# Performance work log

Hardware: AMD Instinct MI355X
Metric: run time of the kernel (lower is better)

The kernel has to match this reference:

```python
import jax, jax.numpy as jnp
import numpy as np

D = 512
HEADS = 4
DIM_HEAD = 128
SCALE = DIM_HEAD ** -0.5
A_NUMS = 60
N_NUMS = 60
DEPTH = 2


def _layer_norm(x, g, b, eps=1e-5):
    m = jnp.mean(x, axis=-1, keepdims=True)
    v = jnp.var(x, axis=-1, keepdims=True)
    return (x - m) * jax.lax.rsqrt(v + eps) * g + b


def _attention(x, qkv_w, out_w, out_b):
    B, T, _ = x.shape
    qkv = x @ qkv_w  # [B,T,3*H*Dh]
    q, k, v = jnp.split(qkv, 3, axis=-1)
    to_heads = lambda t: t.reshape(B, T, HEADS, DIM_HEAD).transpose(0, 2, 1, 3)
    q, k, v = to_heads(q), to_heads(k), to_heads(v)
    att = jax.nn.softmax(jnp.einsum('bhid,bhjd->bhij', q, k) * SCALE, axis=-1)
    o = jnp.einsum('bhij,bhjd->bhid', att, v).transpose(0, 2, 1, 3).reshape(B, T, HEADS * DIM_HEAD)
    return o @ out_w + out_b


def _memory(x, mem, nums):
    # sigmoid similarity to memory slots, topk-mean temporal score, weighted readout
    att = jax.nn.sigmoid(jnp.einsum('btd,kd->btk', x, mem) / jnp.sqrt(jnp.float32(D)))
    vals, _ = jax.lax.top_k(att, nums // 16 + 1)
    temporal_att = vals.mean(-1)  # [B,T]
    aug = jnp.einsum('btk,kd->btd', att, mem)
    return temporal_att, aug


def _topk_gather_mean(att, feats, k):
    _, idx = jax.lax.top_k(att, k)  # [B,k]
    g = jnp.take_along_axis(feats, idx[:, :, None], axis=1)  # [B,k,D]
    return g.mean(1), idx


def _l2norm(x):
    return x / jnp.linalg.norm(x, axis=-1, keepdims=True)


def setup_inputs():
    key = jax.random.key(0)
    ks = jax.random.split(key, 12)
    b, t, din = 64, 256, 1024
    s = 0.02
    return {
        'x': jax.random.normal(ks[0], (b, t, din), jnp.float32),
        'epsilon': jax.random.normal(ks[1], (b // 2, t, D), jnp.float32),
        'conv_w': jax.random.normal(ks[2], (D, din, 3), jnp.float32) * s,
        'conv_b': jnp.zeros((D,), jnp.float32),
        'ln1_g': jnp.ones((DEPTH, D), jnp.float32),
        'ln1_b': jnp.zeros((DEPTH, D), jnp.float32),
        'qkv_w': jax.random.normal(ks[3], (DEPTH, D, 3 * HEADS * DIM_HEAD), jnp.float32) * s,
        'out_w': jax.random.normal(ks[4], (DEPTH, HEADS * DIM_HEAD, D), jnp.float32) * s,
        'out_b': jnp.zeros((DEPTH, D), jnp.float32),
        'ln2_g': jnp.ones((DEPTH, D), jnp.float32),
        'ln2_b': jnp.zeros((DEPTH, D), jnp.float32),
        'ff1_w': jax.random.normal(ks[5], (DEPTH, D, D), jnp.float32) * s,
        'ff1_b': jnp.zeros((DEPTH, D), jnp.float32),
        'ff2_w': jax.random.normal(ks[6], (DEPTH, D, D), jnp.float32) * s,
        'ff2_b': jnp.zeros((DEPTH, D), jnp.float32),
        'a_mem': jax.random.normal(ks[7], (A_NUMS, D), jnp.float32) * s,
        'n_mem': jax.random.normal(ks[8], (N_NUMS, D), jnp.float32) * s,
        'mu_w': jax.random.normal(ks[9], (D, D), jnp.float32) * s,
        'mu_b': jnp.zeros((D,), jnp.float32),
        'var_w': jax.random.normal(ks[10], (D, D), jnp.float32) * s,
        'var_b': jnp.zeros((D,), jnp.float32),
    }


def reference(x, epsilon, conv_w, conv_b, ln1_g, ln1_b, qkv_w, out_w, out_b,
              ln2_g, ln2_b, ff1_w, ff1_b, ff2_w, ff2_b, a_mem, n_mem,
              mu_w, mu_b, var_w, var_b):
    b, t, _ = x.shape
    # Temporal embedding: Conv1d(k=3, pad=1) + ReLU
    h = jax.lax.conv_general_dilated(x.transpose(0, 2, 1), conv_w, (1,), [(1, 1)],
                                     dimension_numbers=('NCH', 'OIH', 'NCH'))
    h = jax.nn.relu(h + conv_b[None, :, None]).transpose(0, 2, 1)  # [B,T,512]
    # Transformer: PreNorm attn + PreNorm FF, residual, depth=2
    for i in range(DEPTH):
        h = h + _attention(_layer_norm(h, ln1_g[i], ln1_b[i]), qkv_w[i], out_w[i], out_b[i])
        f = _layer_norm(h, ln2_g[i], ln2_b[i])
        f = jax.nn.gelu(f @ ff1_w[i] + ff1_b[i], approximate=False)
        h = h + f @ ff2_w[i] + ff2_b[i]
    x_emb = h
    v_feat = x_emb.transpose(0, 2, 1)
    half = b // 2
    N_x, A_x = x_emb[:half], x_emb[half:]
    A_att, A_aug = _memory(A_x, a_mem, A_NUMS)
    N_Aatt, N_Aaug = _memory(A_x, n_mem, N_NUMS)
    A_Natt, A_Naug = _memory(N_x, a_mem, A_NUMS)
    N_att, N_aug = _memory(N_x, n_mem, N_NUMS)
    k = t // 16 + 1
    negative_ax, A_idx = _topk_gather_mean(A_att, A_x, k)
    anchor_nx, N_idx = _topk_gather_mean(N_att, N_x, k)
    positive_nx, _ = _topk_gather_mean(N_Aatt, A_x, k)
    eps = 1e-6
    an, ap, ng = _l2norm(anchor_nx), _l2norm(positive_nx), _l2norm(negative_ax)
    dp = jnp.linalg.norm(an - ap + eps, axis=-1)
    dn = jnp.linalg.norm(an - ng + eps, axis=-1)
    triplet = jnp.mean(jax.nn.relu(dp - dn + 1.0))
    N_aug_mu = N_aug @ mu_w + mu_b
    N_aug_var = N_aug @ var_w + var_b
    N_aug_new = N_aug_mu + epsilon * jnp.sqrt(jnp.exp(N_aug_var))
    anchor_nx_new = jnp.take_along_axis(N_aug_new, N_idx[:, :, None], axis=1).mean(1)
    A_aug_new = A_aug @ mu_w + mu_b
    negative_ax_new = jnp.take_along_axis(A_aug_new, A_idx[:, :, None], axis=1).mean(1)
    kl_loss = jnp.mean(-0.5 * jnp.sum(1.0 + N_aug_var - N_aug_mu ** 2 - jnp.exp(N_aug_var), axis=1))
    A_Naug_m = A_Naug @ mu_w + mu_b
    N_Aaug_m = N_Aaug @ mu_w + mu_b
    na = jnp.maximum(jnp.linalg.norm(anchor_nx, axis=1), eps)
    nn_ = jnp.maximum(jnp.linalg.norm(negative_ax, axis=1), eps)
    cos_loss = jnp.mean(1.0 - jnp.sum(anchor_nx * negative_ax, axis=1) / (na * nn_))
    distance = jnp.mean(jax.nn.relu(100.0 - jnp.linalg.norm(negative_ax_new, axis=-1)
                                    + jnp.linalg.norm(anchor_nx_new, axis=-1)))
    aug_cat = jnp.concatenate([N_aug_new + A_Naug_m, A_aug_new + N_Aaug_m], axis=0)
    x_out = jnp.concatenate([x_emb, aug_cat], axis=-1)  # [B,T,1024]
    return (triplet, kl_loss, distance, A_att, N_att, A_Natt, N_Aatt, cos_loss, x_out, v_feat)
```

## Files before the change

kernel.cpp:

```cpp
#include <hip/hip_runtime.h>
#include <math.h>

namespace {

typedef unsigned short u16;
typedef __attribute__((ext_vector_type(8))) short s8v;
typedef __attribute__((ext_vector_type(8))) unsigned short u16x8;
typedef __attribute__((ext_vector_type(4))) unsigned short u16x4;
typedef __attribute__((ext_vector_type(4))) float f32x4;
typedef __attribute__((ext_vector_type(4))) unsigned int u32x4;

constexpr int HBT = 8192;
constexpr long HHf = 4194304;

constexpr long F_H    = 0;
constexpr long F_LNB  = 8388608;
constexpr long F_QKV  = 12582912;
constexpr long F_VT   = 25165824;
constexpr long F_SC   = 29360128;
constexpr long F_ATT  = 12582912;
constexpr long F_AUG  = 14548992;
constexpr long F_MU   = 22937600;
constexpr long F_VAR  = 27131904;
constexpr long F_R0   = 31326208;
constexpr long F_R1   = 35520512;
constexpr long F_R2   = 39714816;
constexpr long W_MEMB = 43909120;
constexpr long Z_PG   = 43974656;
constexpr long W_QKV  = 46137344;
constexpr long W_OUT  = 46923776;
constexpr long W_FF1  = 47185920;
constexpr long W_FF2  = 47448064;
constexpr long W_MU   = 47710208;
constexpr long W_VAR  = 47841280;
constexpr long W_CONV = 47972352;
constexpr long W_AMT  = 48758784;
constexpr long W_NMT  = 48775168;
constexpr long O_ANC  = 48791552;
constexpr long O_POS  = O_ANC + 16384;
constexpr long O_NEG  = O_POS + 16384;
constexpr long O_ANEW = O_NEG + 16384;
constexpr long O_NNEG = O_ANEW + 16384;
constexpr long O_IDX  = O_NNEG + 16384;
constexpr long O_ACC  = O_IDX + 1632;

constexpr long OO_AATT  = 3;
constexpr long OO_NATT  = 3 + 8192;
constexpr long OO_ANATT = 3 + 16384;
constexpr long OO_NAATT = 3 + 24576;
constexpr long OO_COS   = 32771;
constexpr long OO_XOUT  = 32772;
constexpr long OO_VFEAT = 32772L + 16777216L;

__device__ inline u16 to_bf16(float f) {
  union { float f; unsigned u; } x; x.f = f;
  unsigned r = x.u + 0x7fffu + ((x.u >> 16) & 1u);
  return (u16)(r >> 16);
}
__device__ inline u16x8 pack8(float4 a, float4 b) {
  u16x8 r;
  r[0]=to_bf16(a.x); r[1]=to_bf16(a.y); r[2]=to_bf16(a.z); r[3]=to_bf16(a.w);
  r[4]=to_bf16(b.x); r[5]=to_bf16(b.y); r[6]=to_bf16(b.z); r[7]=to_bf16(b.w);
  return r;
}

typedef __attribute__((address_space(1))) void gvoid;
typedef __attribute__((address_space(3))) void lvoid;
__device__ inline void gld16(const u16* g, u16* l) {
  __builtin_amdgcn_global_load_lds((gvoid*)g, (lvoid*)l, 16, 0, 0);
}

__device__ inline float bred_sum(float v, float* sm, int tid) {
  sm[tid] = v; __syncthreads();
  for (int s = 128; s > 0; s >>= 1) { if (tid < s) sm[tid] += sm[tid + s]; __syncthreads(); }
  float r = sm[0]; __syncthreads();
  return r;
}

struct GP2 {
  const void* A; const void* B; const float* bias; void* C;
  const float* bias2;
  int M, N, K, lda, ldb, ldc, Hdiv;
  long sAb, sAh, sBb, sBh, sCb, sCh;
  float scale;
};


template<int EPI, bool ABF, bool BBF, bool ACC, bool CBF, bool GL>
__global__ __launch_bounds__(256) void mgemm_k(GP2 p) {
  __shared__ __align__(16) u16 As[4096];
  __shared__ __align__(16) u16 Bs[4096];
  int bb = blockIdx.z / p.Hdiv, hh = blockIdx.z % p.Hdiv;
  long aoff = (long)bb * p.sAb + (long)hh * p.sAh;
  long boff = (long)bb * p.sBb + (long)hh * p.sBh;
  long coff = (long)bb * p.sCb + (long)hh * p.sCh;
  int m0 = blockIdx.x * 128, n0 = blockIdx.y * 128;
  int tid = threadIdx.x, r = tid & 127, seg = tid >> 7;
  int lane = tid & 63, wave = tid >> 6;
  int wm = (wave >> 1) * 64, wn = (wave & 1) * 64;
  int l15 = lane & 15, quad = lane >> 4;
  int rs = (r >> 1) & 3;
  int qs = (quad ^ ((l15 >> 1) & 3)) * 8;
  f32x4 acc[4][4] = {};
  for (int k0 = 0; k0 < p.K; k0 += 32) {
    if constexpr (GL) {
      int lr = lane >> 2;
      int lc = (((lane & 3) ^ ((lane >> 3) & 3)) * 8);
      const u16* Ab = (const u16*)p.A + aoff + (long)(m0 + wave * 16 + lr) * p.lda + k0 + lc;
      gld16(Ab,                    &As[wave * 512]);
      gld16(Ab + (long)64 * p.lda, &As[2048 + wave * 512]);
      const u16* Bb = (const u16*)p.B + boff + (long)(n0 + wave * 16 + lr) * p.ldb + k0 + lc;
      gld16(Bb,                    &Bs[wave * 512]);
      gld16(Bb + (long)64 * p.ldb, &Bs[2048 + wave * 512]);
    } else {
      bool kfull = (k0 + 32 <= p.K);
      int p0 = ((2 * seg) ^ rs) * 8;
      int p1 = ((2 * seg + 1) ^ rs) * 8;
      {
        int gm = m0 + r;
        if (ABF) {
          const u16* Ar = (const u16*)p.A + aoff + (long)gm * p.lda + k0 + seg * 16;
          if (kfull) {
            *(u32x4*)&As[r * 32 + p0] = *(const u32x4*)Ar;
            *(u32x4*)&As[r * 32 + p1] = *(const u32x4*)(Ar + 8);
          } else {
            for (int c = 0; c < 16; c++) {
              int kk = k0 + seg * 16 + c;
              int cc = seg * 16 + c;
              As[r * 32 + (((cc >> 3) ^ rs) << 3) + (cc & 7)] = (kk < p.K) ? Ar[c] : (u16)0;
            }
          }
        } else {
          const float* Ar = (const float*)p.A + aoff + (long)gm * p.lda + k0 + seg * 16;
          if (kfull) {
            float4 f0 = ((const float4*)Ar)[0];
            float4 f1 = ((const float4*)Ar)[1];
            float4 f2 = ((const float4*)Ar)[2];
            float4 f3 = ((const float4*)Ar)[3];
            *(u16x8*)&As[r * 32 + p0] = pack8(f0, f1);
            *(u16x8*)&As[r * 32 + p1] = pack8(f2, f3);
          } else {
            for (int c = 0; c < 16; c++) {
              int kk = k0 + seg * 16 + c;
              int cc = seg * 16 + c;
              As[r * 32 + (((cc >> 3) ^ rs) << 3) + (cc & 7)] = (kk < p.K) ? to_bf16(Ar[c]) : (u16)0;
            }
          }
        }
      }
      {
        int gn = n0 + r;
        bool nv = gn < p.N;
        if (BBF) {
          const u16* Br = (const u16*)p.B + boff + (long)gn * p.ldb + k0 + seg * 16;
          if (nv && kfull) {
            *(u32x4*)&Bs[r * 32 + p0] = *(const u32x4*)Br;
            *(u32x4*)&Bs[r * 32 + p1] = *(const u32x4*)(Br + 8);
          } else {
            for (int c = 0; c < 16; c++) {
              int kk = k0 + seg * 16 + c;
              int cc = seg * 16 + c;
              Bs[r * 32 + (((cc >> 3) ^ rs) << 3) + (cc & 7)] = (nv && kk < p.K) ? Br[c] : (u16)0;
            }
          }
        } else {
          const float* Br = (const float*)p.B + boff + (long)gn * p.ldb + k0 + seg * 16;
          if (nv && kfull) {
            float4 f0 = ((const float4*)Br)[0];
            float4 f1 = ((const float4*)Br)[1];
            float4 f2 = ((const float4*)Br)[2];
            float4 f3 = ((const float4*)Br)[3];
            *(u16x8*)&Bs[r * 32 + p0] = pack8(f0, f1);
            *(u16x8*)&Bs[r * 32 + p1] = pack8(f2, f3);
          } else {
            for (int c = 0; c < 16; c++) {
              int kk = k0 + seg * 16 + c;
              int cc = seg * 16 + c;
              Bs[r * 32 + (((cc >> 3) ^ rs) << 3) + (cc & 7)] = (nv && kk < p.K) ? to_bf16(Br[c]) : (u16)0;
            }
          }
        }
      }
    }
    __syncthreads();
    s8v af[4], bfr[4];
#pragma unroll
    for (int i = 0; i < 4; i++) af[i]  = *(const s8v*)&As[(wm + i * 16 + l15) * 32 + qs];
#pragma unroll
    for (int j = 0; j < 4; j++) bfr[j] = *(const s8v*)&Bs[(wn + j * 16 + l15) * 32 + qs];
#pragma unroll
    for (int i = 0; i < 4; i++)
#pragma unroll
      for (int j = 0; j < 4; j++)
        acc[i][j] = __builtin_amdgcn_mfma_f32_16x16x32_bf16(af[i], bfr[j], acc[i][j], 0, 0, 0);
    __syncthreads();
  }
  const float* bp = (p.bias2 && (hh & 1)) ? p.bias2 : p.bias;
#pragma unroll
  for (int j = 0; j < 4; j++) {
    int col = n0 + wn + j * 16 + l15;
    if (col >= p.N) continue;
    float bv = bp ? bp[col] : 0.f;
#pragma unroll
    for (int i = 0; i < 4; i++) {
#pragma unroll
      for (int rr = 0; rr < 4; rr++) {
        int row = m0 + wm + i * 16 + quad * 4 + rr;
        float v = acc[i][j][rr] * p.scale + bv;
        if (EPI == 1) v = 0.5f * v * (1.f + erff(v * 0.70710678118654752f));
        if (EPI == 2) v = 1.f / (1.f + expf(-v));
        long ci = coff + (long)row * p.ldc + col;
        if (CBF) ((u16*)p.C)[ci] = to_bf16(v);
        else {
          float* Cp = (float*)p.C;
          if (ACC) v += Cp[ci];
          Cp[ci] = v;
        }
      }
    }
  }
}

__global__ __launch_bounds__(256) void convm_k(const u16* __restrict__ xb,
    const u16* __restrict__ zp, const u16* __restrict__ wT,
    const float* __restrict__ bias, float* __restrict__ out) {
  __shared__ __align__(16) u16 As[4096];
  __shared__ __align__(16) u16 Bs[4096];
  int m0 = blockIdx.x * 128, n0 = blockIdx.y * 128;
  int b = m0 >> 8, tb = m0 & 255;
  int tid = threadIdx.x;
  int lane = tid & 63, wave = tid >> 6;
  int wm = (wave >> 1) * 64, wn = (wave & 1) * 64;
  int l15 = lane & 15, quad = lane >> 4;
  int lr = lane >> 2;
  int lc = (((lane & 3) ^ ((lane >> 3) & 3)) * 8);
  int qs = (quad ^ ((l15 >> 1) & 3)) * 8;
  int arow = wave * 16 + lr;
  f32x4 acc[4][4] = {};
  for (int k0 = 0; k0 < 3072; k0 += 32) {
    int kp = k0 >> 10, i0 = (k0 & 1023);
    int t2a = tb + arow + kp - 1;
    const u16* Aa = (t2a >= 0 && t2a < 256)
        ? xb + ((long)(b * 256 + t2a)) * 1024 + i0 + lc
        : zp + lc;
    gld16(Aa, &As[wave * 512]);
    int t2b = t2a + 64;
    const u16* Ab2 = (t2b >= 0 && t2b < 256)
        ? xb + ((long)(b * 256 + t2b)) * 1024 + i0 + lc
        : zp + lc;
    gld16(Ab2, &As[2048 + wave * 512]);
    const u16* Bb = wT + (long)(n0 + arow) * 3072 + k0 + lc;
    gld16(Bb,                   &Bs[wave * 512]);
    gld16(Bb + (long)64 * 3072, &Bs[2048 + wave * 512]);
    __syncthreads();
    s8v af[4], bfr[4];
#pragma unroll
    for (int i = 0; i < 4; i++) af[i]  = *(const s8v*)&As[(wm + i * 16 + l15) * 32 + qs];
#pragma unroll
    for (int j = 0; j < 4; j++) bfr[j] = *(const s8v*)&Bs[(wn + j * 16 + l15) * 32 + qs];
#pragma unroll
    for (int i = 0; i < 4; i++)
#pragma unroll
      for (int j = 0; j < 4; j++)
        acc[i][j] = __builtin_amdgcn_mfma_f32_16x16x32_bf16(af[i], bfr[j], acc[i][j], 0, 0, 0);
    __syncthreads();
  }
#pragma unroll
  for (int j = 0; j < 4; j++) {
    int col = n0 + wn + j * 16 + l15;
    float bv = bias[col];
#pragma unroll
    for (int i = 0; i < 4; i++)
#pragma unroll
      for (int rr = 0; rr < 4; rr++) {
        int row = m0 + wm + i * 16 + quad * 4 + rr;
        float v = acc[i][j][rr] + bv;
        out[(long)row * 512 + col] = v > 0.f ? v : 0.f;
      }
  }
}

__global__ __launch_bounds__(256) void wtrans_k(const float* __restrict__ src,
    u16* __restrict__ dst, int R, int C) {
  __shared__ float t[32][33];
  int c0 = blockIdx.x * 32, r0 = blockIdx.y * 32;
  int tx = threadIdx.x & 31, ty = threadIdx.x >> 5;
  for (int rr = 0; rr < 32; rr += 8)
    t[ty + rr][tx] = src[(long)(r0 + ty + rr) * C + c0 + tx];
  __syncthreads();
  for (int rr = 0; rr < 32; rr += 8)
    dst[(long)(c0 + ty + rr) * R + r0 + tx] = to_bf16(t[tx][ty + rr]);
}

struct WT8 { const float* s[8]; long doff[8]; };
__global__ __launch_bounds__(256) void wt8_k(WT8 w, u16* __restrict__ base) {
  __shared__ float t[32][33];
  int z = blockIdx.z;
  const float* src = w.s[z];
  u16* dst = base + w.doff[z];
  int c0 = blockIdx.x * 32, r0 = blockIdx.y * 32;
  int tx = threadIdx.x & 31, ty = threadIdx.x >> 5;
  for (int rr = 0; rr < 32; rr += 8)
    t[ty + rr][tx] = src[(long)(r0 + ty + rr) * 512 + c0 + tx];
  __syncthreads();
  for (int rr = 0; rr < 32; rr += 8)
    dst[(long)(c0 + ty + rr) * 512 + r0 + tx] = to_bf16(t[tx][ty + rr]);
}

__global__ __launch_bounds__(256) void convw_t(const float* __restrict__ src, u16* __restrict__ dst) {
  int id = blockIdx.x * 256 + threadIdx.x;
  if (id >= 512 * 3072) return;
  int o = id / 3072, r2 = id % 3072;
  int kp = r2 >> 10, i = r2 & 1023;
  dst[id] = to_bf16(src[(long)o * 3072 + i * 3 + kp]);
}

__global__ __launch_bounds__(256) void memtrans2_k(const float* __restrict__ a,
    const float* __restrict__ n, u16* __restrict__ amt, u16* __restrict__ nmt) {
  int id = blockIdx.x * 256 + threadIdx.x;
  if (id >= 512 * 64) return;
  const float* src = blockIdx.y ? n : a;
  u16* dst = blockIdx.y ? nmt : amt;
  int nn = id >> 6, k = id & 63;
  dst[id] = (k < 60) ? to_bf16(src[(long)k * 512 + nn]) : (u16)0;
}

__global__ __launch_bounds__(256) void membpad_k(const float* __restrict__ a,
    const float* __restrict__ n, u16* __restrict__ dst) {
  int id = blockIdx.x * 256 + threadIdx.x;
  int mat = id >> 16, r2 = id & 65535;
  int nr = r2 >> 9, k = r2 & 511;
  const float* s = mat ? n : a;
  dst[id] = (nr < 60) ? to_bf16(s[(long)nr * 512 + k]) : (u16)0;
}

__global__ __launch_bounds__(256) void vtrans_k(const u16* __restrict__ qkv, u16* __restrict__ vt) {
  __shared__ u16 t[32][33];
  int z = blockIdx.z;
  int b = z >> 2, h2 = z & 3;
  int t0 = blockIdx.x * 32, d0 = blockIdx.y * 32;
  int tx = threadIdx.x & 31, ty = threadIdx.x >> 5;
  const u16* src = qkv + (long)b * 393216 + 1024 + h2 * 128;
  for (int rr = 0; rr < 32; rr += 8)
    t[ty + rr][tx] = src[(long)(t0 + ty + rr) * 1536 + d0 + tx];
  __syncthreads();
  u16* dst = vt + (long)z * 32768;
  for (int rr = 0; rr < 32; rr += 8)
    dst[(long)(d0 + ty + rr) * 256 + t0 + tx] = t[tx][ty + rr];
}

__global__ __launch_bounds__(256) void cvt_k(const float* __restrict__ src, u16* __restrict__ dst, long n) {
  long i = ((long)blockIdx.x * 256 + threadIdx.x) * 8;
  if (i >= n) return;
  float4 f0 = ((const float4*)(src + i))[0];
  float4 f1 = ((const float4*)(src + i))[1];
  *(u16x8*)(dst + i) = pack8(f0, f1);
}

__global__ void zpage_k(u16* __restrict__ z) { z[threadIdx.x] = 0; }

__global__ __launch_bounds__(256) void ln_k(const float* __restrict__ in,
    const float* __restrict__ g, const float* __restrict__ b, u16* __restrict__ out) {
  int wave = threadIdx.x >> 6, lane = threadIdx.x & 63;
  long row = (long)blockIdx.x * 4 + wave;
  const float* r = in + row * 512 + lane * 8;
  float4 x0 = ((const float4*)r)[0];
  float4 x1 = ((const float4*)r)[1];
  float s = x0.x + x0.y + x0.z + x0.w + x1.x + x1.y + x1.z + x1.w;
  for (int off = 32; off; off >>= 1) s += __shfl_xor(s, off);
  float mean = s * (1.f / 512.f);
  float d[8] = {x0.x - mean, x0.y - mean, x0.z - mean, x0.w - mean,
                x1.x - mean, x1.y - mean, x1.z - mean, x1.w - mean};
  float q = 0.f;
#pragma unroll
  for (int i = 0; i < 8; i++) q += d[i] * d[i];
  for (int off = 32; off; off >>= 1) q += __shfl_xor(q, off);
  float inv = rsqrtf(q * (1.f / 512.f) + 1e-5f);
  const float4* gp = (const float4*)(g + lane * 8);
  const float4* bp = (const float4*)(b + lane * 8);
  float4 g0 = gp[0], g1 = gp[1], b0 = bp[0], b1 = bp[1];
  float gv[8] = {g0.x, g0.y, g0.z, g0.w, g1.x, g1.y, g1.z, g1.w};
  float bv[8] = {b0.x, b0.y, b0.z, b0.w, b1.x, b1.y, b1.z, b1.w};
  u16x8 o;
#pragma unroll
  for (int i = 0; i < 8; i++) o[i] = to_bf16(d[i] * inv * gv[i] + bv[i]);
  *(u16x8*)(out + row * 512 + lane * 8) = o;
}

__global__ __launch_bounds__(256) void softmax_k(const float* __restrict__ s, u16* __restrict__ d) {
  int wave = threadIdx.x >> 6, lane = threadIdx.x & 63;
  long row = (long)blockIdx.x * 4 + wave;
  const float* r = s + row * 256 + lane * 4;
  float4 v = *(const float4*)r;
  float mx = fmaxf(fmaxf(v.x, v.y), fmaxf(v.z, v.w));
  for (int off = 32; off; off >>= 1) mx = fmaxf(mx, __shfl_xor(mx, off));
  v.x = expf(v.x - mx); v.y = expf(v.y - mx); v.z = expf(v.z - mx); v.w = expf(v.w - mx);
  float sum = v.x + v.y + v.z + v.w;
  for (int off = 32; off; off >>= 1) sum += __shfl_xor(sum, off);
  float is = 1.f / sum;
  u16x4 o;
  o[0] = to_bf16(v.x * is); o[1] = to_bf16(v.y * is);
  o[2] = to_bf16(v.z * is); o[3] = to_bf16(v.w * is);
  *(u16x4*)(d + row * 256 + lane * 4) = o;
}

__global__ __launch_bounds__(256) void top4_k(const float* __restrict__ att, float* __restrict__ out) {
  int y = blockIdx.y;
  int i = blockIdx.x * 256 + threadIdx.x;
  if (i >= HBT) return;
  const float* a = att + (long)y * 491520 + (long)i * 60;
  float t0 = -1e30f, t1 = -1e30f, t2 = -1e30f, t3 = -1e30f;
  for (int k = 0; k < 60; k++) {
    float v = a[k];
    if (v > t0)      { t3 = t2; t2 = t1; t1 = t0; t0 = v; }
    else if (v > t1) { t3 = t2; t2 = t1; t1 = v; }
    else if (v > t2) { t3 = t2; t2 = v; }
    else if (v > t3) { t3 = v; }
  }
  int ooff = (y == 0) ? 0 : (4 - y) * 8192;
  out[ooff + i] = (t0 + t1 + t2 + t3) * 0.25f;
}

__global__ __launch_bounds__(256) void topk17_k(const float* __restrict__ tatt, int* __restrict__ idx) {
  int b = blockIdx.x, y = blockIdx.y, tid = threadIdx.x;
  __shared__ float sv[256];
  __shared__ int si[256];
  float v = tatt[(long)y * 8192 + (long)b * 256 + tid];
  int* ob = idx + y * 544 + b * 17;
  for (int s = 0; s < 17; s++) {
    sv[tid] = v; si[tid] = tid;
    __syncthreads();
    for (int off = 128; off > 0; off >>= 1) {
      if (tid < off) {
        float v2 = sv[tid + off]; int i2 = si[tid + off];
        if (v2 > sv[tid] || (v2 == sv[tid] && i2 < si[tid])) { sv[tid] = v2; si[tid] = i2; }
      }
      __syncthreads();
    }
    int win = si[0];
    if (tid == 0) ob[s] = win;
    if (tid == win) v = -1e30f;
    __syncthreads();
  }
}

__device__ inline void gmean_body(const float* feats, const int* idx, float* out, int b, int tid) {
  float s0 = 0.f, s1 = 0.f;
  for (int j = 0; j < 17; j++) {
    int t = idx[b * 17 + j];
    const float* r = feats + ((long)b * 256 + t) * 512;
    s0 += r[tid]; s1 += r[tid + 256];
  }
  out[(long)b * 512 + tid]       = s0 * (1.f / 17.f);
  out[(long)b * 512 + tid + 256] = s1 * (1.f / 17.f);
}

__global__ __launch_bounds__(256) void gmean3_k(const float* __restrict__ Ax,
    const float* __restrict__ Nx, const int* __restrict__ idx0, float* __restrict__ ob) {
  int b = blockIdx.x, y = blockIdx.y, tid = threadIdx.x;
  const float* feats = (y == 1) ? Nx : Ax;
  const int* idx = idx0 + y * 544;
  float* out = ob + (long)((y + 2) % 3) * 16384;
  gmean_body(feats, idx, out, b, tid);
}

__global__ __launch_bounds__(256) void gmean2_k(const float* __restrict__ f0,
    const float* __restrict__ f1, const int* __restrict__ idx0, float* __restrict__ ob) {
  int b = blockIdx.x, y = blockIdx.y, tid = threadIdx.x;
  const float* feats = y ? f1 : f0;
  const int* idx = idx0 + (y == 0 ? 544 : 0);
  float* out = ob + (long)y * 16384;
  gmean_body(feats, idx, out, b, tid);
}

__global__ __launch_bounds__(256) void vae_k(const float* __restrict__ mu,
    const float* __restrict__ var, const float* __restrict__ eps,
    float* __restrict__ nnew, float* __restrict__ accum) {
  constexpr long N4 = HHf / 4;
  long stride = (long)gridDim.x * 256;
  float kle = 0.f;
  for (long i = (long)blockIdx.x * 256 + threadIdx.x; i < N4; i += stride) {
    float4 m4 = ((const float4*)mu)[i];
    float4 v4 = ((const float4*)var)[i];
    float4 e4 = ((const float4*)eps)[i];
    float4 o;
    float ev;
    ev = expf(v4.x); o.x = m4.x + e4.x * sqrtf(ev); kle += 1.f + v4.x - m4.x * m4.x - ev;
    ev = expf(v4.y); o.y = m4.y + e4.y * sqrtf(ev); kle += 1.f + v4.y - m4.y * m4.y - ev;
    ev = expf(v4.z); o.z = m4.z + e4.z * sqrtf(ev); kle += 1.f + v4.z - m4.z * m4.z - ev;
    ev = expf(v4.w); o.w = m4.w + e4.w * sqrtf(ev); kle += 1.f + v4.w - m4.w * m4.w - ev;
    ((float4*)nnew)[i] = o;
  }
  __shared__ float sm[256];
  float s = bred_sum(kle, sm, threadIdx.x);
  if (threadIdx.x == 0) atomicAdd(accum + 0, s);
}

__global__ __launch_bounds__(256) void tripcos_k(const float* __restrict__ anc,
    const float* __restrict__ pos, const float* __restrict__ neg, float* __restrict__ accum) {
  int b = blockIdx.x, tid = threadIdx.x;
  const float *a = anc + (long)b * 512, *p = pos + (long)b * 512, *n = neg + (long)b * 512;
  float a0 = a[tid], a1 = a[tid + 256], p0 = p[tid], p1 = p[tid + 256], n0 = n[tid], n1 = n[tid + 256];
  __shared__ float sm[256];
  float sa  = bred_sum(a0 * a0 + a1 * a1, sm, tid);
  float sp  = bred_sum(p0 * p0 + p1 * p1, sm, tid);
  float sn  = bred_sum(n0 * n0 + n1 * n1, sm, tid);
  float dot = bred_sum(a0 * n0 + a1 * n1, sm, tid);
  float na = sqrtf(sa), np_ = sqrtf(sp), nn = sqrtf(sn);
  float ina = 1.f / na, inp = 1.f / np_, inn = 1.f / nn;
  float d0 = a0 * ina - p0 * inp + 1e-6f, d1 = a1 * ina - p1 * inp + 1e-6f;
  float e0 = a0 * ina - n0 * inn + 1e-6f, e1 = a1 * ina - n1 * inn + 1e-6f;
  float dp2 = bred_sum(d0 * d0 + d1 * d1, sm, tid);
  float dn2 = bred_sum(e0 * e0 + e1 * e1, sm, tid);
  if (tid == 0) {
    float dp = sqrtf(dp2), dn = sqrtf(dn2);
    float t = dp - dn + 1.f;
    atomicAdd(accum + 1, t > 0.f ? t : 0.f);
    float c = 1.f - dot / (fmaxf(na, 1e-6f) * fmaxf(nn, 1e-6f));
    atomicAdd(accum + 2, c);
  }
}

__global__ __launch_bounds__(256) void dist_k(const float* __restrict__ anew,
    const float* __restrict__ nneg, float* __restrict__ accum) {
  int b = blockIdx.x, tid = threadIdx.x;
  const float *a = anew + (long)b * 512, *n = nneg + (long)b * 512;
  float a0 = a[tid], a1 = a[tid + 256], n0 = n[tid], n1 = n[tid + 256];
  __shared__ float sm[256];
  float sa = bred_sum(a0 * a0 + a1 * a1, sm, tid);
  float sn = bred_sum(n0 * n0 + n1 * n1, sm, tid);
  if (tid == 0) {
    float v = 100.f - sqrtf(sn) + sqrtf(sa);
    atomicAdd(accum + 3, v > 0.f ? v : 0.f);
  }
}

__global__ __launch_bounds__(256) void xout_k(const float* __restrict__ emb,
    const float* __restrict__ nnew, const float* __restrict__ anm,
    const float* __restrict__ anew, const float* __restrict__ nam,
    float* __restrict__ xout) {
  long i = (long)blockIdx.x * 256 + threadIdx.x;
  long row = i >> 9;
  int d = (int)(i & 511);
  long o = row * 1024 + d;
  xout[o] = emb[i];
  float v;
  if (i < HHf) v = nnew[i] + anm[i];
  else         v = anew[i - HHf] + nam[i - HHf];
  xout[o + 512] = v;
}

__global__ __launch_bounds__(256) void vfeat_k(const float* __restrict__ emb, float* __restrict__ vf) {
  __shared__ float tile[32][33];
  int b = blockIdx.z;
  int t0 = blockIdx.x * 32, d0 = blockIdx.y * 32;
  int tx = threadIdx.x & 31, ty = threadIdx.x >> 5;
  for (int r = 0; r < 32; r += 8)
    tile[ty + r][tx] = emb[((long)b * 256 + t0 + ty + r) * 512 + d0 + tx];
  __syncthreads();
  for (int r = 0; r < 32; r += 8)
    vf[((long)b * 512 + d0 + ty + r) * 256 + t0 + tx] = tile[tx][ty + r];
}

__global__ void init_k(float* accum) {
  accum[0] = 0.f; accum[1] = 0.f; accum[2] = 0.f; accum[3] = 0.f;
}

__global__ void fin_k(const float* __restrict__ accum, float* __restrict__ out) {
  out[0] = accum[1] * (1.f / 32.f);
  out[1] = -0.5f * accum[0] * (1.f / 16384.f);
  out[2] = accum[3] * (1.f / 32.f);
  out[OO_COS] = accum[2] * (1.f / 32.f);
}

static inline GP2 mk(const void* A, const void* B, const float* bias, void* C,
                     int M, int N, int K, int lda, int ldb, int ldc,
                     float scale = 1.f, int Hdiv = 1,
                     long sAb = 0, long sAh = 0, long sBb = 0, long sBh = 0,
                     long sCb = 0, long sCh = 0, const float* bias2 = nullptr) {
  GP2 p; p.A = A; p.B = B; p.bias = bias; p.C = C; p.bias2 = bias2;
  p.M = M; p.N = N; p.K = K; p.lda = lda; p.ldb = ldb; p.ldc = ldc;
  p.Hdiv = Hdiv; p.sAb = sAb; p.sAh = sAh; p.sBb = sBb; p.sBh = sBh;
  p.sCb = sCb; p.sCh = sCh; p.scale = scale;
  return p;
}

}

extern "C" void kernel_launch(void* const* d_in, const int* in_sizes, int n_in,
                              void* d_out, int out_size, void* d_ws, size_t ws_size,
                              hipStream_t stream) {
  const float* x      = (const float*)d_in[0];
  const float* epsi   = (const float*)d_in[1];
  const float* conv_w = (const float*)d_in[2];
  const float* conv_b = (const float*)d_in[3];
  const float* ln1_g  = (const float*)d_in[4];
  const float* ln1_b  = (const float*)d_in[5];
  const float* qkv_w  = (const float*)d_in[6];
  const float* out_w  = (const float*)d_in[7];
  const float* out_b  = (const float*)d_in[8];
  const float* ln2_g  = (const float*)d_in[9];
  const float* ln2_b  = (const float*)d_in[10];
  const float* ff1_w  = (const float*)d_in[11];
  const float* ff1_b  = (const float*)d_in[12];
  const float* ff2_w  = (const float*)d_in[13];
  const float* ff2_b  = (const float*)d_in[14];
  const float* a_mem  = (const float*)d_in[15];
  const float* n_mem  = (const float*)d_in[16];
  const float* mu_w   = (const float*)d_in[17];
  const float* mu_b   = (const float*)d_in[18];
  const float* var_w  = (const float*)d_in[19];
  const float* var_b  = (const float*)d_in[20];
  float* out = (float*)d_out;
  float* ws  = (float*)d_ws;

  const float ATTSCALE = 0.08838834764831845f;
  const float SIGSCALE = 0.04419417382415922f;

  float* h   = ws + F_H;
  u16* lnb   = (u16*)(ws + F_LNB);
  u16* qkvb  = (u16*)(ws + F_QKV);
  u16* vtb   = (u16*)(ws + F_VT);
  float* scf = ws + F_SC;
  u16* scb   = qkvb;
  u16* wqkvT = (u16*)(ws + W_QKV);
  u16* woutT = (u16*)(ws + W_OUT);
  u16* wff1T = (u16*)(ws + W_FF1);
  u16* wff2T = (u16*)(ws + W_FF2);
  u16* wmuT  = (u16*)(ws + W_MU);
  u16* wconvT= (u16*)(ws + W_CONV);
  u16* amtT  = (u16*)(ws + W_AMT);
  u16* nmtT  = (u16*)(ws + W_NMT);
  u16* membT = (u16*)(ws + W_MEMB);
  u16* zpage = (u16*)(ws + Z_PG);
  u16* xb    = (u16*)(ws + F_QKV);

  wtrans_k<<<dim3(48, 16), 256, 0, stream>>>(qkv_w,          wqkvT,          512, 1536);
  wtrans_k<<<dim3(48, 16), 256, 0, stream>>>(qkv_w + 786432, wqkvT + 786432, 512, 1536);
  {
    WT8 w;
    w.s[0] = out_w;          w.doff[0] = 2 * W_OUT;
    w.s[1] = out_w + 262144; w.doff[1] = 2 * W_OUT + 262144;
    w.s[2] = ff1_w;          w.doff[2] = 2 * W_FF1;
    w.s[3] = ff1_w + 262144; w.doff[3] = 2 * W_FF1 + 262144;
    w.s[4] = ff2_w;          w.doff[4] = 2 * W_FF2;
    w.s[5] = ff2_w + 262144; w.doff[5] = 2 * W_FF2 + 262144;
    w.s[6] = mu_w;           w.doff[6] = 2 * W_MU;
    w.s[7] = var_w;          w.doff[7] = 2 * W_VAR;
    wt8_k<<<dim3(16, 16, 8), 256, 0, stream>>>(w, (u16*)ws);
  }
  convw_t<<<6144, 256, 0, stream>>>(conv_w, wconvT);
  memtrans2_k<<<dim3(128, 2), 256, 0, stream>>>(a_mem, n_mem, amtT, nmtT);

  cvt_k<<<8192, 256, 0, stream>>>(x, xb, 16777216);
  zpage_k<<<1, 256, 0, stream>>>(zpage);
  convm_k<<<dim3(128, 4), 256, 0, stream>>>(xb, zpage, wconvT, conv_b, h);

  for (int i = 0; i < 2; i++) {
    ln_k<<<4096, 256, 0, stream>>>(h, ln1_g + i * 512, ln1_b + i * 512, lnb);
    {
      GP2 p = mk(lnb, wqkvT + (long)i * 786432, nullptr, qkvb, 16384, 1536, 512, 512, 512, 1536);
      mgemm_k<0, true, true, false, true, true><<<dim3(128, 12, 1), 256, 0, stream>>>(p);
    }
    vtrans_k<<<dim3(8, 4, 256), 256, 0, stream>>>(qkvb, vtb);
    {
      GP2 p = mk(qkvb, qkvb + 512, nullptr, scf, 256, 256, 128, 1536, 1536, 256,
                 ATTSCALE, 4, 393216, 128, 393216, 128, 262144, 65536);
      mgemm_k<0, true, true, false, false, true><<<dim3(2, 2, 256), 256, 0, stream>>>(p);
    }
    softmax_k<<<16384, 256, 0, stream>>>(scf, scb);
    {
      GP2 p = mk(scb, vtb, nullptr, lnb, 256, 128, 256, 256, 256, 512,
                 1.f, 4, 262144, 65536, 131072, 32768, 131072, 128);
      mgemm_k<0, true, true, false, true, true><<<dim3(2, 1, 256), 256, 0, stream>>>(p);
    }
    {
      GP2 p = mk(lnb, woutT + (long)i * 262144, out_b + i * 512, h, 16384, 512, 512, 512, 512, 512);
      mgemm_k<0, true, true, true, false, true><<<dim3(128, 4, 1), 256, 0, stream>>>(p);
    }
    ln_k<<<4096, 256, 0, stream>>>(h, ln2_g + i * 512, ln2_b + i * 512, lnb);
    {
      GP2 p = mk(lnb, wff1T + (long)i * 262144, ff1_b + i * 512, qkvb, 16384, 512, 512, 512, 512, 512);
      mgemm_k<1, true, true, false, true, true><<<dim3(128, 4, 1), 256, 0, stream>>>(p);
    }
    {
      GP2 p = mk(qkvb, wff2T + (long)i * 262144, ff2_b + i * 512, h, 16384, 512, 512, 512, 512, 512);
      mgemm_k<0, true, true, true, false, true><<<dim3(128, 4, 1), 256, 0, stream>>>(p);
    }
  }

  u16* hb = lnb;
  cvt_k<<<4096, 256, 0, stream>>>(h, hb, 8388608);
  membpad_k<<<512, 256, 0, stream>>>(a_mem, n_mem, membT);
  const float* Nx = h;
  const float* Ax = h + HHf;
  const u16* Axb = hb + HHf;
  float* attA  = ws + F_ATT;
  float* attN  = ws + F_ATT + 1474560;

  {
    GP2 p = mk(Axb, membT, nullptr, attA, HBT, 60, 512, 512, 512, 60, SIGSCALE,
               2, -(long)HHf, 0, 0, 65536, 983040, 491520);
    mgemm_k<2, true, true, false, false, true><<<dim3(64, 1, 4), 256, 0, stream>>>(p);
  }

  top4_k<<<dim3(32, 4), 256, 0, stream>>>(attA, out + OO_AATT);

  u16* augb = (u16*)(ws + F_AUG);
  u16* augA  = augb;
  u16* augN  = augb + 3 * HHf;
  {
    GP2 p = mk(attA, amtT, nullptr, augA, HBT, 512, 60, 60, 64, 512, 1.f,
               2, 983040, 491520, 0, 32768, 2 * HHf, HHf);
    mgemm_k<0, false, true, false, true, false><<<dim3(64, 4, 4), 256, 0, stream>>>(p);
  }

  float* accum = ws + O_ACC;
  int* idxA = (int*)(ws + O_IDX);
  init_k<<<1, 1, 0, stream>>>(accum);

  topk17_k<<<dim3(32, 3), 256, 0, stream>>>(out + OO_AATT, idxA);
  gmean3_k<<<dim3(32, 3), 256, 0, stream>>>(Ax, Nx, idxA, ws + O_ANC);
  tripcos_k<<<32, 256, 0, stream>>>(ws + O_ANC, ws + O_POS, ws + O_NEG, accum);

  {
    GP2 p = mk(augN, wmuT, mu_b, ws + F_MU, HBT, 512, 512, 512, 512, 512, 1.f,
               2, 0, 0, 0, 262144, 0, 4194304, var_b);
    mgemm_k<0, true, true, false, false, true><<<dim3(64, 4, 2), 256, 0, stream>>>(p);
  }
  vae_k<<<512, 256, 0, stream>>>(ws + F_MU, ws + F_VAR, epsi, ws + F_MU, accum);

  {
    GP2 p = mk(augA, wmuT, mu_b, ws + F_R0, HBT, 512, 512, 512, 512, 512, 1.f,
               1, HHf, 0, 0, 0, 4194304, 0);
    mgemm_k<0, true, true, false, false, true><<<dim3(64, 4, 3), 256, 0, stream>>>(p);
  }

  gmean2_k<<<dim3(32, 2), 256, 0, stream>>>(ws + F_MU, ws + F_R0, idxA, ws + O_ANEW);
  dist_k<<<32, 256, 0, stream>>>(ws + O_ANEW, ws + O_NNEG, accum);

  xout_k<<<32768, 256, 0, stream>>>(h, ws + F_MU, ws + F_R2, ws + F_R0, ws + F_R1,
                                    out + OO_XOUT);
  vfeat_k<<<dim3(8, 16, 64), 256, 0, stream>>>(h, out + OO_VFEAT);
  fin_k<<<1, 1, 0, stream>>>(accum, out);
}
```

Measured before the change: 962.0 us.

## Double-buffer LDS tiles in async-load GEMM and conv kernels

Adds a second LDS buffer for the direct global-to-LDS load paths in the GEMM kernel and the conv GEMM. The next K-tile is prefetched while MFMAs run on the current tile, which removes one barrier per iteration. The aim is to hide global load latency behind compute. In exchange, LDS per block doubles to 32KB, including on the non-GL path that does not use the extra space, which may reduce occupancy.

```diff
diff --git a/kernel.cpp b/kernel.cpp
--- a/kernel.cpp
+++ b/kernel.cpp
@@ -88,8 +88,8 @@
 
 template<int EPI, bool ABF, bool BBF, bool ACC, bool CBF, bool GL>
 __global__ __launch_bounds__(256) void mgemm_k(GP2 p) {
-  __shared__ __align__(16) u16 As[4096];
-  __shared__ __align__(16) u16 Bs[4096];
+  __shared__ __align__(16) u16 As[8192];
+  __shared__ __align__(16) u16 Bs[8192];
   int bb = blockIdx.z / p.Hdiv, hh = blockIdx.z % p.Hdiv;
   long aoff = (long)bb * p.sAb + (long)hh * p.sAh;
   long boff = (long)bb * p.sBb + (long)hh * p.sBh;
@@ -102,17 +102,37 @@
   int rs = (r >> 1) & 3;
   int qs = (quad ^ ((l15 >> 1) & 3)) * 8;
   f32x4 acc[4][4] = {};
-  for (int k0 = 0; k0 < p.K; k0 += 32) {
-    if constexpr (GL) {
-      int lr = lane >> 2;
-      int lc = (((lane & 3) ^ ((lane >> 3) & 3)) * 8);
-      const u16* Ab = (const u16*)p.A + aoff + (long)(m0 + wave * 16 + lr) * p.lda + k0 + lc;
-      gld16(Ab,                    &As[wave * 512]);
-      gld16(Ab + (long)64 * p.lda, &As[2048 + wave * 512]);
-      const u16* Bb = (const u16*)p.B + boff + (long)(n0 + wave * 16 + lr) * p.ldb + k0 + lc;
-      gld16(Bb,                    &Bs[wave * 512]);
-      gld16(Bb + (long)64 * p.ldb, &Bs[2048 + wave * 512]);
-    } else {
+  if constexpr (GL) {
+    int lr = lane >> 2;
+    int lc = (((lane & 3) ^ ((lane >> 3) & 3)) * 8);
+    const u16* Abase = (const u16*)p.A + aoff + (long)(m0 + wave * 16 + lr) * p.lda + lc;
+    const u16* Bbase = (const u16*)p.B + boff + (long)(n0 + wave * 16 + lr) * p.ldb + lc;
+    auto stage = [&](int buf, int k0) {
+      gld16(Abase + k0,                    &As[buf * 4096 + wave * 512]);
+      gld16(Abase + k0 + (long)64 * p.lda, &As[buf * 4096 + 2048 + wave * 512]);
+      gld16(Bbase + k0,                    &Bs[buf * 4096 + wave * 512]);
+      gld16(Bbase + k0 + (long)64 * p.ldb, &Bs[buf * 4096 + 2048 + wave * 512]);
+    };
+    stage(0, 0);
+    __syncthreads();
+    int cur = 0;
+    for (int k0 = 0; k0 < p.K; k0 += 32) {
+      if (k0 + 32 < p.K) stage(cur ^ 1, k0 + 32);
+      s8v af[4], bfr[4];
+#pragma unroll
+      for (int i = 0; i < 4; i++) af[i]  = *(const s8v*)&As[cur * 4096 + (wm + i * 16 + l15) * 32 + qs];
+#pragma unroll
+      for (int j = 0; j < 4; j++) bfr[j] = *(const s8v*)&Bs[cur * 4096 + (wn + j * 16 + l15) * 32 + qs];
+#pragma unroll
+      for (int i = 0; i < 4; i++)
+#pragma unroll
+        for (int j = 0; j < 4; j++)
+          acc[i][j] = __builtin_amdgcn_mfma_f32_16x16x32_bf16(af[i], bfr[j], acc[i][j], 0, 0, 0);
+      __syncthreads();
+      cur ^= 1;
+    }
+  } else {
+    for (int k0 = 0; k0 < p.K; k0 += 32) {
       bool kfull = (k0 + 32 <= p.K);
       int p0 = ((2 * seg) ^ rs) * 8;
       int p1 = ((2 * seg + 1) ^ rs) * 8;
@@ -181,19 +201,19 @@
           }
         }
       }
-    }
-    __syncthreads();
-    s8v af[4], bfr[4];
-#pragma unroll
-    for (int i = 0; i < 4; i++) af[i]  = *(const s8v*)&As[(wm + i * 16 + l15) * 32 + qs];
-#pragma unroll
-    for (int j = 0; j < 4; j++) bfr[j] = *(const s8v*)&Bs[(wn + j * 16 + l15) * 32 + qs];
-#pragma unroll
-    for (int i = 0; i < 4; i++)
-#pragma unroll
-      for (int j = 0; j < 4; j++)
-        acc[i][j] = __builtin_amdgcn_mfma_f32_16x16x32_bf16(af[i], bfr[j], acc[i][j], 0, 0, 0);
-    __syncthreads();
+      __syncthreads();
+      s8v af[4], bfr[4];
+#pragma unroll
+      for (int i = 0; i < 4; i++) af[i]  = *(const s8v*)&As[(wm + i * 16 + l15) * 32 + qs];
+#pragma unroll
+      for (int j = 0; j < 4; j++) bfr[j] = *(const s8v*)&Bs[(wn + j * 16 + l15) * 32 + qs];
+#pragma unroll
+      for (int i = 0; i < 4; i++)
+#pragma unroll
+        for (int j = 0; j < 4; j++)
+          acc[i][j] = __builtin_amdgcn_mfma_f32_16x16x32_bf16(af[i], bfr[j], acc[i][j], 0, 0, 0);
+      __syncthreads();
+    }
   }
   const float* bp = (p.bias2 && (hh & 1)) ? p.bias2 : p.bias;
 #pragma unroll
@@ -224,8 +244,8 @@
 __global__ __launch_bounds__(256) void convm_k(const u16* __restrict__ xb,
     const u16* __restrict__ zp, const u16* __restrict__ wT,
     const float* __restrict__ bias, float* __restrict__ out) {
-  __shared__ __align__(16) u16 As[4096];
-  __shared__ __align__(16) u16 Bs[4096];
+  __shared__ __align__(16) u16 As[8192];
+  __shared__ __align__(16) u16 Bs[8192];
   int m0 = blockIdx.x * 128, n0 = blockIdx.y * 128;
   int b = m0 >> 8, tb = m0 & 255;
   int tid = threadIdx.x;
@@ -237,33 +257,39 @@
   int qs = (quad ^ ((l15 >> 1) & 3)) * 8;
   int arow = wave * 16 + lr;
   f32x4 acc[4][4] = {};
-  for (int k0 = 0; k0 < 3072; k0 += 32) {
+  auto stage = [&](int buf, int k0) {
     int kp = k0 >> 10, i0 = (k0 & 1023);
     int t2a = tb + arow + kp - 1;
     const u16* Aa = (t2a >= 0 && t2a < 256)
         ? xb + ((long)(b * 256 + t2a)) * 1024 + i0 + lc
         : zp + lc;
-    gld16(Aa, &As[wave * 512]);
+    gld16(Aa, &As[buf * 4096 + wave * 512]);
     int t2b = t2a + 64;
     const u16* Ab2 = (t2b >= 0 && t2b < 256)
         ? xb + ((long)(b * 256 + t2b)) * 1024 + i0 + lc
         : zp + lc;
-    gld16(Ab2, &As[2048 + wave * 512]);
+    gld16(Ab2, &As[buf * 4096 + 2048 + wave * 512]);
     const u16* Bb = wT + (long)(n0 + arow) * 3072 + k0 + lc;
-    gld16(Bb,                   &Bs[wave * 512]);
-    gld16(Bb + (long)64 * 3072, &Bs[2048 + wave * 512]);
-    __syncthreads();
+    gld16(Bb,                   &Bs[buf * 4096 + wave * 512]);
+    gld16(Bb + (long)64 * 3072, &Bs[buf * 4096 + 2048 + wave * 512]);
+  };
+  stage(0, 0);
+  __syncthreads();
+  int cur = 0;
+  for (int k0 = 0; k0 < 3072; k0 += 32) {
+    if (k0 + 32 < 3072) stage(cur ^ 1, k0 + 32);
     s8v af[4], bfr[4];
 #pragma unroll
-    for (int i = 0; i < 4; i++) af[i]  = *(const s8v*)&As[(wm + i * 16 + l15) * 32 + qs];
-#pragma unroll
-    for (int j = 0; j < 4; j++) bfr[j] = *(const s8v*)&Bs[(wn + j * 16 + l15) * 32 + qs];
+    for (int i = 0; i < 4; i++) af[i]  = *(const s8v*)&As[cur * 4096 + (wm + i * 16 + l15) * 32 + qs];
+#pragma unroll
+    for (int j = 0; j < 4; j++) bfr[j] = *(const s8v*)&Bs[cur * 4096 + (wn + j * 16 + l15) * 32 + qs];
 #pragma unroll
     for (int i = 0; i < 4; i++)
 #pragma unroll
       for (int j = 0; j < 4; j++)
         acc[i][j] = __builtin_amdgcn_mfma_f32_16x16x32_bf16(af[i], bfr[j], acc[i][j], 0, 0, 0);
     __syncthreads();
+    cur ^= 1;
   }
 #pragma unroll
   for (int j = 0; j < 4; j++) {
```

After: 1.063 ms. 10.5% more time.
